# Optimization experiments

Measured on AMD Instinct MI355X. Metric: run time of the kernel, lower is better.

Reference implementation:

```python
import jax, jax.numpy as jnp
import numpy as np

B, N, D = 32, 64, 256

def _gelu(x):
    return jax.nn.gelu(x, approximate=False)

def setup_inputs() -> dict:
    key = jax.random.key(0)
    ks = jax.random.split(key, 16)
    def w(k, shape):
        fan_in = shape[0]
        return (jax.random.normal(k, shape, jnp.float32) / np.float32(np.sqrt(fan_in)))
    return {
        "dataset_embedding": jax.random.normal(ks[0], (B, D), jnp.float32),
        "variable_embeddings": jax.random.normal(ks[1], (B, N, D), jnp.float32),
        "claim_context": jax.random.normal(ks[2], (B, D), jnp.float32),
        "dge_w1": w(ks[3], (2 * D, D)), "dge_b1": jnp.zeros((D,), jnp.float32),
        "dge_w2": w(ks[4], (D, D)),     "dge_b2": jnp.zeros((D,), jnp.float32),
        "cge_w1": w(ks[5], (2 * D, D)), "cge_b1": jnp.zeros((D,), jnp.float32),
        "cge_w2": w(ks[6], (D, D)),     "cge_b2": jnp.zeros((D,), jnp.float32),
        "dep_w1": w(ks[7], (4 * D, D)), "dep_b1": jnp.zeros((D,), jnp.float32),
        "dep_w2": w(ks[8], (D, 1)),     "dep_b2": jnp.zeros((1,), jnp.float32),
        "cep_w1": w(ks[9], (4 * D, D)), "cep_b1": jnp.zeros((D,), jnp.float32),
        "cep_w2": w(ks[10], (D, 1)),    "cep_b2": jnp.zeros((1,), jnp.float32),
        "gate_w1": w(ks[11], (3, 64)),  "gate_b1": jnp.zeros((64,), jnp.float32),
        "gate_w2": w(ks[12], (64, 1)),  "gate_b2": jnp.zeros((1,), jnp.float32),
        "n_samples": 500,
    }

def _encode(ve, ctx, w1, b1, w2, b2):
    # Sequential(Linear(2d,d), GELU, Linear(d,d), GELU); dropout=0 (eval)
    x = jnp.concatenate([ve, jnp.broadcast_to(ctx[:, None, :], ve.shape)], axis=-1)
    h = _gelu(x @ w1 + b1)
    return _gelu(h @ w2 + b2)

def _predict_edges(ve_enc, ctx, w1, b1, w2, b2):
    # var_with_context: [B,N,2D]; edge features cat([var_i, var_j]) @ w1
    # == (vwc @ w1[:2D]) broadcast over i + (vwc @ w1[2D:]) broadcast over j
    vwc = jnp.concatenate([ve_enc, jnp.broadcast_to(ctx[:, None, :], ve_enc.shape)], axis=-1)
    wi, wj = w1[: 2 * D], w1[2 * D :]
    fi = vwc @ wi  # [B,N,D]
    fj = vwc @ wj  # [B,N,D]
    h = _gelu(fi[:, :, None, :] + fj[:, None, :, :] + b1)  # [B,N,N,D]
    logits = jnp.einsum("bijd,do->bij", h, w2) + b2[0]
    eye = jnp.eye(N, dtype=bool)
    return jnp.where(eye[None, :, :], jnp.float32(-1e9), logits)

def reference(dataset_embedding, variable_embeddings, claim_context,
              dge_w1, dge_b1, dge_w2, dge_b2,
              cge_w1, cge_b1, cge_w2, cge_b2,
              dep_w1, dep_b1, dep_w2, dep_b2,
              cep_w1, cep_b1, cep_w2, cep_b2,
              gate_w1, gate_b1, gate_w2, gate_b2,
              n_samples):
    avg_claim_confidence = 0.5
    var_data = _encode(variable_embeddings, dataset_embedding, dge_w1, dge_b1, dge_w2, dge_b2)
    var_claim = _encode(variable_embeddings, claim_context, cge_w1, cge_b1, cge_w2, cge_b2)
    W_data_logits = _predict_edges(var_data, dataset_embedding, dep_w1, dep_b1, dep_w2, dep_b2)
    W_claim_logits = _predict_edges(var_claim, claim_context, cep_w1, cep_b1, cep_w2, cep_b2)

    p = jax.nn.sigmoid(W_data_logits)
    eps = jnp.float32(1e-8)
    data_entropy = -(p * jnp.log(p + eps) + (1 - p) * jnp.log(1 - p + eps)).mean(axis=(1, 2))  # [B]

    ns = jnp.full((B,), min(n_samples / 1000.0, 1.0), jnp.float32)
    cc = jnp.full((B,), avg_claim_confidence, jnp.float32)
    gf = jnp.stack([ns, cc, data_entropy], axis=-1)  # [B,3]
    gate = jax.nn.sigmoid(_gelu(gf @ gate_w1 + gate_b1) @ gate_w2 + gate_b2)  # [B,1]
    gate = gate[:, :, None]  # [B,1,1]

    W_post_logits = gate * W_data_logits + (1 - gate) * W_claim_logits

    # NOTEARS: h(W) = tr(expm(W o W)) - n, W = sigmoid(logits)
    Wsig = jax.nn.sigmoid(W_post_logits)
    M = jax.vmap(jax.scipy.linalg.expm)(Wsig * Wsig)
    acyc = (jnp.trace(M, axis1=1, axis2=2) - N).mean()

    W_posterior = jax.nn.sigmoid(W_post_logits)
    return (W_posterior, acyc)
```

## Files before the change

### kernel.cpp

```cpp
#include <hip/hip_runtime.h>
#include <hip/hip_bf16.h>


#define LDS_STRIDE 260
#define ES 68

__device__ __forceinline__ float gelu_f(float x) {
    float z = fabsf(x) * 0.70710678118654752440f;
    float t = __builtin_amdgcn_rcpf(fmaf(0.3275911f, z, 1.0f));
    float p = t * fmaf(t, fmaf(t, fmaf(t, fmaf(t, 1.061405429f, -1.453152027f),
                                       1.421413741f), -0.284496736f), 0.254829592f);
    float e = __expf(-z * z);
    float erfv = fmaf(-p, e, 1.0f);
    erfv = copysignf(erfv, x);
    return 0.5f * x * (1.0f + erfv);
}
__device__ __forceinline__ float sigmoid_f(float x) {
    return 1.0f / (1.0f + expf(-x));
}
__device__ __forceinline__ float f4c(const float4& v, int k) {
    return k == 0 ? v.x : k == 1 ? v.y : k == 2 ? v.z : v.w;
}
__device__ __forceinline__ float4 ld4(const float* __restrict__ buf, int r, int c) {
    return *(const float4*)&buf[r * ES + c];
}

__global__ __launch_bounds__(256) void k0_ctx(
    const float* __restrict__ ds, const float* __restrict__ cc,
    const float* __restrict__ dge_w1, const float* __restrict__ dge_b1,
    const float* __restrict__ cge_w1, const float* __restrict__ cge_b1,
    const float* __restrict__ dep_w1, const float* __restrict__ dep_b1,
    const float* __restrict__ cep_w1, const float* __restrict__ cep_b1,
    float* __restrict__ ctxproj)
{
    const int b = blockIdx.x;
    const int which = blockIdx.y;
    const float* ctx; const float* W; const float* bias;
    switch (which) {
        case 0:  ctx = ds; W = dge_w1 + 256 * 256; bias = dge_b1; break;
        case 1:  ctx = cc; W = cge_w1 + 256 * 256; bias = cge_b1; break;
        case 2:  ctx = ds; W = dep_w1 + 256 * 256; bias = dep_b1; break;
        case 3:  ctx = ds; W = dep_w1 + 768 * 256; bias = nullptr; break;
        case 4:  ctx = cc; W = cep_w1 + 256 * 256; bias = cep_b1; break;
        default: ctx = cc; W = cep_w1 + 768 * 256; bias = nullptr; break;
    }
    __shared__ float sctx[256];
    const int tid = threadIdx.x;
    sctx[tid] = ctx[b * 256 + tid];
    __syncthreads();
    float acc = 0.0f;
    #pragma unroll 2
    for (int k = 0; k < 256; k += 4) {
        float4 c4 = *(const float4*)&sctx[k];
        acc = fmaf(c4.x, W[(k + 0) * 256 + tid], acc);
        acc = fmaf(c4.y, W[(k + 1) * 256 + tid], acc);
        acc = fmaf(c4.z, W[(k + 2) * 256 + tid], acc);
        acc = fmaf(c4.w, W[(k + 3) * 256 + tid], acc);
    }
    if (bias) acc += bias[tid];
    ctxproj[(which * 32 + b) * 256 + tid] = acc;
}

__device__ __forceinline__ void gemm_ks(const float* __restrict__ src,
                                        const float* __restrict__ W,
                                        int ks0, int t0, float acc[8][4])
{
    #pragma unroll
    for (int r = 0; r < 8; ++r)
        #pragma unroll
        for (int c = 0; c < 4; ++c) acc[r][c] = 0.0f;
    #pragma unroll 2
    for (int k = ks0; k < ks0 + 32; k += 4) {
        float4 wv0 = *(const float4*)&W[(k + 0) * 256 + t0];
        float4 wv1 = *(const float4*)&W[(k + 1) * 256 + t0];
        float4 wv2 = *(const float4*)&W[(k + 2) * 256 + t0];
        float4 wv3 = *(const float4*)&W[(k + 3) * 256 + t0];
        float4 a[8];
        #pragma unroll
        for (int r = 0; r < 8; ++r) a[r] = *(const float4*)&src[r * LDS_STRIDE + k];
        float4 wvs[4] = {wv0, wv1, wv2, wv3};
        #pragma unroll
        for (int kk = 0; kk < 4; ++kk) {
            float4 wv = wvs[kk];
            #pragma unroll
            for (int r = 0; r < 8; ++r) {
                float av = f4c(a[r], kk);
                acc[r][0] = fmaf(av, wv.x, acc[r][0]);
                acc[r][1] = fmaf(av, wv.y, acc[r][1]);
                acc[r][2] = fmaf(av, wv.z, acc[r][2]);
                acc[r][3] = fmaf(av, wv.w, acc[r][3]);
            }
        }
    }
}

__device__ __forceinline__ void part_write_rmw(float* __restrict__ part, int w, int t0,
                                               const float acc[8][4])
{
    if (w < 4) {
        #pragma unroll
        for (int r = 0; r < 8; ++r) {
            float4 o = {acc[r][0], acc[r][1], acc[r][2], acc[r][3]};
            *(float4*)&part[(w * 8 + r) * 256 + t0] = o;
        }
    }
    __syncthreads();
    if (w >= 4) {
        #pragma unroll
        for (int r = 0; r < 8; ++r) {
            float4 v = *(const float4*)&part[((w - 4) * 8 + r) * 256 + t0];
            float4 o = {v.x + acc[r][0], v.y + acc[r][1], v.z + acc[r][2], v.w + acc[r][3]};
            *(float4*)&part[((w - 4) * 8 + r) * 256 + t0] = o;
        }
    }
    __syncthreads();
}

__device__ __forceinline__ float4 reduce4(const float* __restrict__ part, int r, int t0)
{
    float4 s = {0.0f, 0.0f, 0.0f, 0.0f};
    #pragma unroll
    for (int sl = 0; sl < 4; ++sl) {
        float4 v = *(const float4*)&part[(sl * 8 + r) * 256 + t0];
        s.x += v.x; s.y += v.y; s.z += v.z; s.w += v.w;
    }
    return s;
}

__global__ __launch_bounds__(512, 4) void k1_encode(
    const float* __restrict__ ve_g,
    const float* __restrict__ dge_w1, const float* __restrict__ dge_w2, const float* __restrict__ dge_b2,
    const float* __restrict__ cge_w1, const float* __restrict__ cge_w2, const float* __restrict__ cge_b2,
    const float* __restrict__ dep_w1, const float* __restrict__ cep_w1,
    const float* __restrict__ ctxproj,
    float* __restrict__ fi_dep, float* __restrict__ fjt_dep,
    float* __restrict__ fi_cep, float* __restrict__ fjt_cep)
{
    __shared__ float sve[8 * LDS_STRIDE];
    __shared__ float sA[8 * LDS_STRIDE];
    __shared__ float sB[8 * LDS_STRIDE];
    __shared__ float part[4 * 8 * 256];

    const int tid   = threadIdx.x;
    const int blk   = blockIdx.x;
    const int chain = blk & 1;
    const int chunk = (blk >> 1) & 7;
    const int b     = blk >> 4;
    const int n0    = chunk * 8;

    const float* w1   = chain ? cge_w1 : dge_w1;
    const float* w2   = chain ? cge_w2 : dge_w2;
    const float* b2   = chain ? cge_b2 : dge_b2;
    const float* epw  = chain ? cep_w1 : dep_w1;
    float* fi  = chain ? fi_cep  : fi_dep;
    float* fjt = chain ? fjt_cep : fjt_dep;
    const int cp_s1 = chain ? 1 : 0;
    const int cp_fi = chain ? 4 : 2;
    const int cp_fj = chain ? 5 : 3;

    const int w  = tid >> 6;
    const int t0 = (tid & 63) * 4;
    const int ks0 = w * 32;

    float4 cp1 = *(const float4*)&ctxproj[(cp_s1 * 32 + b) * 256 + t0];
    float4 bv2 = *(const float4*)&b2[t0];
    float4 cpf = *(const float4*)&ctxproj[(cp_fi * 32 + b) * 256 + t0];
    float4 cpj = *(const float4*)&ctxproj[(cp_fj * 32 + b) * 256 + t0];

    {
        int idx = tid * 4;
        int r = idx >> 8, k = idx & 255;
        *(float4*)&sve[r * LDS_STRIDE + k] = *(const float4*)&ve_g[(b * 64 + n0) * 256 + idx];
    }
    __syncthreads();

    float acc[8][4];

    gemm_ks(sve, w1, ks0, t0, acc);
    part_write_rmw(part, w, t0, acc);
    {
        float4 s = reduce4(part, w, t0);
        float4 o = {gelu_f(s.x + cp1.x), gelu_f(s.y + cp1.y),
                    gelu_f(s.z + cp1.z), gelu_f(s.w + cp1.w)};
        *(float4*)&sA[w * LDS_STRIDE + t0] = o;
    }
    __syncthreads();

    gemm_ks(sA, w2, ks0, t0, acc);
    part_write_rmw(part, w, t0, acc);
    {
        float4 s = reduce4(part, w, t0);
        float4 o = {gelu_f(s.x + bv2.x), gelu_f(s.y + bv2.y),
                    gelu_f(s.z + bv2.z), gelu_f(s.w + bv2.w)};
        *(float4*)&sB[w * LDS_STRIDE + t0] = o;
    }
    __syncthreads();

    gemm_ks(sB, epw, ks0, t0, acc);
    part_write_rmw(part, w, t0, acc);
    {
        float4 s = reduce4(part, w, t0);
        float4 o = {s.x + cpf.x, s.y + cpf.y, s.z + cpf.z, s.w + cpf.w};
        *(float4*)&fi[(b * 64 + n0 + w) * 256 + t0] = o;
    }
    __syncthreads();

    gemm_ks(sB, epw + 512 * 256, ks0, t0, acc);
    part_write_rmw(part, w, t0, acc);
    {
        float4 s = reduce4(part, w, t0);
        float4 o = {s.x + cpj.x, s.y + cpj.y, s.z + cpj.z, s.w + cpj.w};
        *(float4*)&sA[w * LDS_STRIDE + t0] = o;
    }
    __syncthreads();
    {
        int t = tid & 255, half = tid >> 8;
        float v0 = sA[(half * 4 + 0) * LDS_STRIDE + t];
        float v1 = sA[(half * 4 + 1) * LDS_STRIDE + t];
        float v2 = sA[(half * 4 + 2) * LDS_STRIDE + t];
        float v3 = sA[(half * 4 + 3) * LDS_STRIDE + t];
        float4 o = {v0, v1, v2, v3};
        *(float4*)&fjt[(b * 256 + t) * 64 + n0 + half * 4] = o;
    }
}

__global__ __launch_bounds__(512) void k3_edges(
    const float* __restrict__ fi_dep, const float* __restrict__ fjt_dep,
    const float* __restrict__ fi_cep, const float* __restrict__ fjt_cep,
    const float* __restrict__ dep_w2, const float* __restrict__ dep_b2,
    const float* __restrict__ cep_w2, const float* __restrict__ cep_b2,
    float* __restrict__ Wd, float* __restrict__ Wc, float* __restrict__ entp)
{
    __shared__ float fj_s[2][64 * 64];
    __shared__ float fi_s[4][256];
    __shared__ float w2_s[256];
    __shared__ float red[8][64];

    const int blk  = blockIdx.x;
    const int pred = blk & 1;
    const int ig   = (blk >> 1) & 15;
    const int b    = blk >> 5;
    const int tid  = threadIdx.x;
    const int s    = tid >> 6;
    const int j    = tid & 63;
    const int row  = s & 3;
    const int dh   = s >> 2;

    const float* fi_g  = pred ? fi_cep  : fi_dep;
    const float* fjt_g = pred ? fjt_cep : fjt_dep;
    const float* w2_g  = pred ? cep_w2  : dep_w2;
    const float* b2_g  = pred ? cep_b2  : dep_b2;
    float* W_out = pred ? Wc : Wd;

    if (tid < 256) {
        int rr = tid >> 6, c = (tid & 63) * 4;
        *(float4*)&fi_s[rr][c] = *(const float4*)&fi_g[(b * 64 + ig * 4 + rr) * 256 + c];
    } else if (tid < 320) {
        int t = tid - 256;
        *(float4*)&w2_s[t * 4] = *(const float4*)&w2_g[t * 4];
    }

    const float4* gF = (const float4*)(fjt_g + b * 256 * 64);

    float4 r0 = gF[tid], r1 = gF[tid + 512];
    ((float4*)fj_s[0])[tid] = r0; ((float4*)fj_s[0])[tid + 512] = r1;
    __syncthreads();

    float acc = 0.0f;
    const int d0 = dh * 32;

    #pragma unroll
    for (int c = 0; c < 4; ++c) {
        const int p = c & 1;
        if (c < 3) {
            const int off = (c + 1) * 1024;
            r0 = gF[off + tid]; r1 = gF[off + tid + 512];
        }
        const float* fj = fj_s[p];
        const int c0 = c * 64;
        #pragma unroll 4
        for (int d = d0; d < d0 + 32; d += 2) {
            float f0 = fi_s[row][c0 + d];
            float f1 = fi_s[row][c0 + d + 1];
            float g0 = fj[(d + 0) * 64 + j];
            float g1 = fj[(d + 1) * 64 + j];
            acc = fmaf(gelu_f(f0 + g0), w2_s[c0 + d],     acc);
            acc = fmaf(gelu_f(f1 + g1), w2_s[c0 + d + 1], acc);
        }
        if (c < 3) {
            const int q = p ^ 1;
            ((float4*)fj_s[q])[tid] = r0; ((float4*)fj_s[q])[tid + 512] = r1;
            __syncthreads();
        }
    }

    red[s][j] = acc;
    __syncthreads();

    if (s < 4) {
        const int i = ig * 4 + s;
        float l = (red[s][j] + red[s + 4][j]) + b2_g[0];
        if (j == i) l = -1e9f;
        W_out[(b * 64 + i) * 64 + j] = l;

        if (pred == 0) {
            float p = sigmoid_f(l);
            float e = -(p * logf(p + 1e-8f) + (1.0f - p) * logf(1.0f - p + 1e-8f));
            #pragma unroll
            for (int off = 32; off; off >>= 1) e += __shfl_down(e, off);
            if (j == 0) entp[b * 64 + i] = e;
        }
    }
}

__device__ __forceinline__ void mm64f2(const float* __restrict__ A, const float* __restrict__ B,
                                       int r0, int c0, float acc[2][4])
{
    #pragma unroll
    for (int i = 0; i < 2; ++i)
        #pragma unroll
        for (int j = 0; j < 4; ++j) acc[i][j] = 0.0f;
    for (int kb = 0; kb < 64; kb += 4) {
        float4 a0 = ld4(A, r0 + 0, kb);
        float4 a1 = ld4(A, r0 + 1, kb);
        #pragma unroll
        for (int kk = 0; kk < 4; ++kk) {
            float4 rv = ld4(B, kb + kk, c0);
            float x0 = f4c(a0, kk), x1 = f4c(a1, kk);
            acc[0][0] = fmaf(x0, rv.x, acc[0][0]);
            acc[0][1] = fmaf(x0, rv.y, acc[0][1]);
            acc[0][2] = fmaf(x0, rv.z, acc[0][2]);
            acc[0][3] = fmaf(x0, rv.w, acc[0][3]);
            acc[1][0] = fmaf(x1, rv.x, acc[1][0]);
            acc[1][1] = fmaf(x1, rv.y, acc[1][1]);
            acc[1][2] = fmaf(x1, rv.z, acc[1][2]);
            acc[1][3] = fmaf(x1, rv.w, acc[1][3]);
        }
    }
}

__device__ __forceinline__ void mm64d2(const float* __restrict__ A, const float* __restrict__ B,
                                       int r0, int c0, double acc[2][4])
{
    #pragma unroll
    for (int i = 0; i < 2; ++i)
        #pragma unroll
        for (int j = 0; j < 4; ++j) acc[i][j] = 0.0;
    for (int kb = 0; kb < 64; kb += 4) {
        float4 a0 = ld4(A, r0 + 0, kb);
        float4 a1 = ld4(A, r0 + 1, kb);
        #pragma unroll
        for (int kk = 0; kk < 4; ++kk) {
            float4 rv = ld4(B, kb + kk, c0);
            double rj[4] = {(double)rv.x, (double)rv.y, (double)rv.z, (double)rv.w};
            double x0 = (double)f4c(a0, kk), x1 = (double)f4c(a1, kk);
            #pragma unroll
            for (int j = 0; j < 4; ++j) {
                acc[0][j] = fma(x0, rj[j], acc[0][j]);
                acc[1][j] = fma(x1, rj[j], acc[1][j]);
            }
        }
    }
}

__global__ __launch_bounds__(512) void k6_gate_expm(
    const float* __restrict__ Wd, const float* __restrict__ Wc,
    const float* __restrict__ entp,
    const float* __restrict__ gw1, const float* __restrict__ gb1,
    const float* __restrict__ gw2, const float* __restrict__ gb2,
    const int* __restrict__ n_samples,
    float* __restrict__ out, float* __restrict__ traces)
{
    __shared__ float Xs [64 * ES];
    __shared__ float X2s[64 * ES];
    __shared__ float X3s[64 * ES];
    __shared__ float Ra [64 * ES];
    __shared__ float Rb [64 * ES];
    __shared__ float sgate;
    __shared__ float sent;
    __shared__ int ssexp;

    const int b = blockIdx.x;
    const int tid = threadIdx.x;

    const float C2 = 0.5f, C3 = 1.0f/6.0f, C4 = 1.0f/24.0f, C5 = 1.0f/120.0f;
    const float C6 = 1.0f/720.0f, C7 = 1.0f/5040.0f, C8 = 1.0f/40320.0f;
    const float C9 = 1.0f/362880.0f, C10 = 1.0f/3628800.0f, C11 = 1.0f/39916800.0f;
    const float C12 = 1.0f/479001600.0f, C13 = 1.0f/6227020800.0f;

    if (tid < 64) {
        float v = entp[b * 64 + tid];
        #pragma unroll
        for (int off = 32; off; off >>= 1) v += __shfl_down(v, off);
        if (tid == 0) sent = v / 4096.0f;
    }
    __syncthreads();
    if (tid < 64) {
        float ns = fminf((float)n_samples[0] / 1000.0f, 1.0f);
        float ccf = 0.5f;
        float pre = ns * gw1[tid] + ccf * gw1[64 + tid] + sent * gw1[128 + tid] + gb1[tid];
        float hid = gelu_f(pre) * gw2[tid];
        #pragma unroll
        for (int off = 32; off; off >>= 1) hid += __shfl_down(hid, off);
        if (tid == 0) sgate = sigmoid_f(hid + gb2[0]);
    }
    __syncthreads();
    const float g = sgate;

    for (int idx = tid; idx < 4096; idx += 512) {
        float d = Wd[b * 4096 + idx];
        float c = Wc[b * 4096 + idx];
        float post = g * d + (1.0f - g) * c;
        float sg = sigmoid_f(post);
        out[b * 4096 + idx] = sg;
        Xs[(idx >> 6) * ES + (idx & 63)] = sg * sg;
    }
    __syncthreads();

    if (tid < 64) {
        float cs = 0.0f;
        for (int r = 0; r < 64; ++r) cs += Xs[r * ES + tid];
        #pragma unroll
        for (int off = 32; off; off >>= 1) cs = fmaxf(cs, __shfl_down(cs, off));
        if (tid == 0) {
            int se = 0;
            if (cs > 2.0f) se = (int)ceilf(log2f(cs * 0.5f));
            if (se < 0) se = 0;
            if (se > 12) se = 12;
            ssexp = se;
        }
    }
    __syncthreads();
    const int sexp = ssexp;
    const float scale = ldexpf(1.0f, -sexp);
    for (int idx = tid; idx < 4096; idx += 512) {
        Xs[(idx >> 6) * ES + (idx & 63)] *= scale;
    }
    __syncthreads();

    const int r0 = (tid >> 4) * 2;
    const int c0 = (tid & 15) * 4;
    float acc[2][4];

    mm64f2(Xs, Xs, r0, c0, acc);
    #pragma unroll
    for (int i = 0; i < 2; ++i) {
        float4 o = {acc[i][0], acc[i][1], acc[i][2], acc[i][3]};
        *(float4*)&X2s[(r0 + i) * ES + c0] = o;
    }
    __syncthreads();

    mm64f2(X2s, Xs, r0, c0, acc);
    #pragma unroll
    for (int i = 0; i < 2; ++i) {
        float4 o = {acc[i][0], acc[i][1], acc[i][2], acc[i][3]};
        *(float4*)&X3s[(r0 + i) * ES + c0] = o;
    }
    __syncthreads();

    mm64f2(Xs, X3s, r0, c0, acc);
    #pragma unroll
    for (int i = 0; i < 2; ++i) {
        float4 xv = ld4(Xs, r0 + i, c0);
        float4 x2 = ld4(X2s, r0 + i, c0);
        float4 x3 = ld4(X3s, r0 + i, c0);
        float o[4];
        #pragma unroll
        for (int j = 0; j < 4; ++j) {
            o[j] = C13 * acc[i][j] + C12 * f4c(x3, j) + C10 * f4c(xv, j) + C11 * f4c(x2, j)
                 + ((r0 + i) == (c0 + j) ? C9 : 0.0f);
        }
        float4 ov = {o[0], o[1], o[2], o[3]};
        *(float4*)&Ra[(r0 + i) * ES + c0] = ov;
    }
    __syncthreads();

    mm64f2(Ra, X3s, r0, c0, acc);
    #pragma unroll
    for (int i = 0; i < 2; ++i) {
        float4 xv = ld4(Xs, r0 + i, c0);
        float4 x2 = ld4(X2s, r0 + i, c0);
        float o[4];
        #pragma unroll
        for (int j = 0; j < 4; ++j) {
            o[j] = acc[i][j] + C7 * f4c(xv, j) + C8 * f4c(x2, j)
                 + ((r0 + i) == (c0 + j) ? C6 : 0.0f);
        }
        float4 ov = {o[0], o[1], o[2], o[3]};
        *(float4*)&Rb[(r0 + i) * ES + c0] = ov;
    }
    __syncthreads();

    mm64f2(Rb, X3s, r0, c0, acc);
    #pragma unroll
    for (int i = 0; i < 2; ++i) {
        float4 xv = ld4(Xs, r0 + i, c0);
        float4 x2 = ld4(X2s, r0 + i, c0);
        float o[4];
        #pragma unroll
        for (int j = 0; j < 4; ++j) {
            o[j] = acc[i][j] + C4 * f4c(xv, j) + C5 * f4c(x2, j)
                 + ((r0 + i) == (c0 + j) ? C3 : 0.0f);
        }
        float4 ov = {o[0], o[1], o[2], o[3]};
        *(float4*)&Ra[(r0 + i) * ES + c0] = ov;
    }
    __syncthreads();

    mm64f2(Ra, X3s, r0, c0, acc);
    #pragma unroll
    for (int i = 0; i < 2; ++i) {
        float4 xv = ld4(Xs, r0 + i, c0);
        float4 x2 = ld4(X2s, r0 + i, c0);
        float o[4];
        #pragma unroll
        for (int j = 0; j < 4; ++j) {
            o[j] = acc[i][j] + f4c(xv, j) + C2 * f4c(x2, j)
                 + ((r0 + i) == (c0 + j) ? 1.0f : 0.0f);
        }
        float4 ov = {o[0], o[1], o[2], o[3]};
        *(float4*)&Rb[(r0 + i) * ES + c0] = ov;
    }
    __syncthreads();

    float* cur = Rb;
    float* oth = Ra;
    for (int sq = 0; sq < sexp; ++sq) {
        double dacc[2][4];
        mm64d2(cur, cur, r0, c0, dacc);
        #pragma unroll
        for (int i = 0; i < 2; ++i) {
            float4 o = {(float)dacc[i][0], (float)dacc[i][1], (float)dacc[i][2], (float)dacc[i][3]};
            *(float4*)&oth[(r0 + i) * ES + c0] = o;
        }
        __syncthreads();
        float* t = cur; cur = oth; oth = t;
    }

    if (tid < 64) {
        double v = (double)cur[tid * ES + tid];
        #pragma unroll
        for (int off = 32; off; off >>= 1) v += __shfl_down(v, off);
        if (tid == 0) traces[b] = (float)v;
    }
}

__global__ void k7_acyc(const float* __restrict__ traces, float* __restrict__ out)
{
    if (threadIdx.x == 0 && blockIdx.x == 0) {
        double s = 0.0;
        for (int b = 0; b < 32; ++b) s += (double)traces[b];
        out[131072] = (float)(s / 32.0 - 64.0);
    }
}

extern "C" void kernel_launch(void* const* d_in, const int* in_sizes, int n_in,
                              void* d_out, int out_size, void* d_ws, size_t ws_size,
                              hipStream_t stream)
{
    (void)in_sizes; (void)n_in; (void)out_size; (void)ws_size;

    const float* ds     = (const float*)d_in[0];
    const float* ve     = (const float*)d_in[1];
    const float* cc     = (const float*)d_in[2];
    const float* dge_w1 = (const float*)d_in[3];
    const float* dge_b1 = (const float*)d_in[4];
    const float* dge_w2 = (const float*)d_in[5];
    const float* dge_b2 = (const float*)d_in[6];
    const float* cge_w1 = (const float*)d_in[7];
    const float* cge_b1 = (const float*)d_in[8];
    const float* cge_w2 = (const float*)d_in[9];
    const float* cge_b2 = (const float*)d_in[10];
    const float* dep_w1 = (const float*)d_in[11];
    const float* dep_b1 = (const float*)d_in[12];
    const float* dep_w2 = (const float*)d_in[13];
    const float* dep_b2 = (const float*)d_in[14];
    const float* cep_w1 = (const float*)d_in[15];
    const float* cep_b1 = (const float*)d_in[16];
    const float* cep_w2 = (const float*)d_in[17];
    const float* cep_b2 = (const float*)d_in[18];
    const float* gw1    = (const float*)d_in[19];
    const float* gb1    = (const float*)d_in[20];
    const float* gw2    = (const float*)d_in[21];
    const float* gb2    = (const float*)d_in[22];
    const int*   nsamp  = (const int*)d_in[23];

    float* ws = (float*)d_ws;
    float* ctxproj = ws;
    float* fi_dep  = ctxproj + 49152;
    float* fjt_dep = fi_dep + 524288;
    float* fi_cep  = fjt_dep + 524288;
    float* fjt_cep = fi_cep + 524288;
    float* Wd      = fjt_cep + 524288;
    float* Wc      = Wd + 131072;
    float* entp    = Wc + 131072;
    float* traces  = entp + 2048;

    float* outp = (float*)d_out;

    k0_ctx<<<dim3(32, 6), 256, 0, stream>>>(ds, cc, dge_w1, dge_b1, cge_w1, cge_b1,
                                            dep_w1, dep_b1, cep_w1, cep_b1, ctxproj);
    k1_encode<<<512, 512, 0, stream>>>(ve, dge_w1, dge_w2, dge_b2,
                                       cge_w1, cge_w2, cge_b2,
                                       dep_w1, cep_w1, ctxproj,
                                       fi_dep, fjt_dep, fi_cep, fjt_cep);
    k3_edges<<<1024, 512, 0, stream>>>(fi_dep, fjt_dep, fi_cep, fjt_cep,
                                       dep_w2, dep_b2, cep_w2, cep_b2,
                                       Wd, Wc, entp);
    k6_gate_expm<<<32, 512, 0, stream>>>(Wd, Wc, entp, gw1, gb1, gw2, gb2,
                                         nsamp, outp, traces);
    k7_acyc<<<1, 64, 0, stream>>>(traces, outp);
}
```

Measured before the change: 120.8 us.

## Replace split-K encode GEMM with per-thread full-K output tiling

```diff
diff --git a/kernel.cpp b/kernel.cpp
--- a/kernel.cpp
+++ b/kernel.cpp
@@ -61,70 +61,35 @@
     ctxproj[(which * 32 + b) * 256 + tid] = acc;
 }
 
-__device__ __forceinline__ void gemm_ks(const float* __restrict__ src,
+__device__ __forceinline__ void gemm_cs(const float* __restrict__ src,
                                         const float* __restrict__ W,
-                                        int ks0, int t0, float acc[8][4])
-{
-    #pragma unroll
-    for (int r = 0; r < 8; ++r)
-        #pragma unroll
-        for (int c = 0; c < 4; ++c) acc[r][c] = 0.0f;
+                                        int r, int c0, float acc[4])
+{
+    acc[0] = acc[1] = acc[2] = acc[3] = 0.0f;
     #pragma unroll 2
-    for (int k = ks0; k < ks0 + 32; k += 4) {
-        float4 wv0 = *(const float4*)&W[(k + 0) * 256 + t0];
-        float4 wv1 = *(const float4*)&W[(k + 1) * 256 + t0];
-        float4 wv2 = *(const float4*)&W[(k + 2) * 256 + t0];
-        float4 wv3 = *(const float4*)&W[(k + 3) * 256 + t0];
-        float4 a[8];
-        #pragma unroll
-        for (int r = 0; r < 8; ++r) a[r] = *(const float4*)&src[r * LDS_STRIDE + k];
-        float4 wvs[4] = {wv0, wv1, wv2, wv3};
-        #pragma unroll
-        for (int kk = 0; kk < 4; ++kk) {
-            float4 wv = wvs[kk];
-            #pragma unroll
-            for (int r = 0; r < 8; ++r) {
-                float av = f4c(a[r], kk);
-                acc[r][0] = fmaf(av, wv.x, acc[r][0]);
-                acc[r][1] = fmaf(av, wv.y, acc[r][1]);
-                acc[r][2] = fmaf(av, wv.z, acc[r][2]);
-                acc[r][3] = fmaf(av, wv.w, acc[r][3]);
-            }
-        }
-    }
-}
-
-__device__ __forceinline__ void part_write_rmw(float* __restrict__ part, int w, int t0,
-                                               const float acc[8][4])
-{
-    if (w < 4) {
-        #pragma unroll
-        for (int r = 0; r < 8; ++r) {
-            float4 o = {acc[r][0], acc[r][1], acc[r][2], acc[r][3]};
-            *(float4*)&part[(w * 8 + r) * 256 + t0] = o;
-        }
-    }
-    __syncthreads();
-    if (w >= 4) {
-        #pragma unroll
-        for (int r = 0; r < 8; ++r) {
-            float4 v = *(const float4*)&part[((w - 4) * 8 + r) * 256 + t0];
-            float4 o = {v.x + acc[r][0], v.y + acc[r][1], v.z + acc[r][2], v.w + acc[r][3]};
-            *(float4*)&part[((w - 4) * 8 + r) * 256 + t0] = o;
-        }
-    }
-    __syncthreads();
-}
-
-__device__ __forceinline__ float4 reduce4(const float* __restrict__ part, int r, int t0)
-{
-    float4 s = {0.0f, 0.0f, 0.0f, 0.0f};
-    #pragma unroll
-    for (int sl = 0; sl < 4; ++sl) {
-        float4 v = *(const float4*)&part[(sl * 8 + r) * 256 + t0];
-        s.x += v.x; s.y += v.y; s.z += v.z; s.w += v.w;
-    }
-    return s;
+    for (int k = 0; k < 256; k += 4) {
+        float4 a  = *(const float4*)&src[r * LDS_STRIDE + k];
+        float4 w0 = *(const float4*)&W[(k + 0) * 256 + c0];
+        float4 w1 = *(const float4*)&W[(k + 1) * 256 + c0];
+        float4 w2 = *(const float4*)&W[(k + 2) * 256 + c0];
+        float4 w3 = *(const float4*)&W[(k + 3) * 256 + c0];
+        acc[0] = fmaf(a.x, w0.x, acc[0]);
+        acc[1] = fmaf(a.x, w0.y, acc[1]);
+        acc[2] = fmaf(a.x, w0.z, acc[2]);
+        acc[3] = fmaf(a.x, w0.w, acc[3]);
+        acc[0] = fmaf(a.y, w1.x, acc[0]);
+        acc[1] = fmaf(a.y, w1.y, acc[1]);
+        acc[2] = fmaf(a.y, w1.z, acc[2]);
+        acc[3] = fmaf(a.y, w1.w, acc[3]);
+        acc[0] = fmaf(a.z, w2.x, acc[0]);
+        acc[1] = fmaf(a.z, w2.y, acc[1]);
+        acc[2] = fmaf(a.z, w2.z, acc[2]);
+        acc[3] = fmaf(a.z, w2.w, acc[3]);
+        acc[0] = fmaf(a.w, w3.x, acc[0]);
+        acc[1] = fmaf(a.w, w3.y, acc[1]);
+        acc[2] = fmaf(a.w, w3.z, acc[2]);
+        acc[3] = fmaf(a.w, w3.w, acc[3]);
+    }
 }
 
 __global__ __launch_bounds__(512, 4) void k1_encode(
@@ -139,7 +104,6 @@
     __shared__ float sve[8 * LDS_STRIDE];
     __shared__ float sA[8 * LDS_STRIDE];
     __shared__ float sB[8 * LDS_STRIDE];
-    __shared__ float part[4 * 8 * 256];
 
     const int tid   = threadIdx.x;
     const int blk   = blockIdx.x;
@@ -159,60 +123,53 @@
     const int cp_fj = chain ? 5 : 3;
 
     const int w  = tid >> 6;
-    const int t0 = (tid & 63) * 4;
-    const int ks0 = w * 32;
-
-    float4 cp1 = *(const float4*)&ctxproj[(cp_s1 * 32 + b) * 256 + t0];
-    float4 bv2 = *(const float4*)&b2[t0];
-    float4 cpf = *(const float4*)&ctxproj[(cp_fi * 32 + b) * 256 + t0];
-    float4 cpj = *(const float4*)&ctxproj[(cp_fj * 32 + b) * 256 + t0];
+    const int l  = tid & 63;
+    const int r  = l >> 3;
+    const int c0 = w * 32 + (l & 7) * 4;
+
+    float4 cp1 = *(const float4*)&ctxproj[(cp_s1 * 32 + b) * 256 + c0];
+    float4 bv2 = *(const float4*)&b2[c0];
+    float4 cpf = *(const float4*)&ctxproj[(cp_fi * 32 + b) * 256 + c0];
+    float4 cpj = *(const float4*)&ctxproj[(cp_fj * 32 + b) * 256 + c0];
 
     {
         int idx = tid * 4;
-        int r = idx >> 8, k = idx & 255;
-        *(float4*)&sve[r * LDS_STRIDE + k] = *(const float4*)&ve_g[(b * 64 + n0) * 256 + idx];
-    }
-    __syncthreads();
-
-    float acc[8][4];
-
-    gemm_ks(sve, w1, ks0, t0, acc);
-    part_write_rmw(part, w, t0, acc);
+        int rr = idx >> 8, k = idx & 255;
+        *(float4*)&sve[rr * LDS_STRIDE + k] = *(const float4*)&ve_g[(b * 64 + n0) * 256 + idx];
+    }
+    __syncthreads();
+
+    float acc[4];
+
+    gemm_cs(sve, w1, r, c0, acc);
     {
-        float4 s = reduce4(part, w, t0);
-        float4 o = {gelu_f(s.x + cp1.x), gelu_f(s.y + cp1.y),
-                    gelu_f(s.z + cp1.z), gelu_f(s.w + cp1.w)};
-        *(float4*)&sA[w * LDS_STRIDE + t0] = o;
-    }
-    __syncthreads();
-
-    gemm_ks(sA, w2, ks0, t0, acc);
-    part_write_rmw(part, w, t0, acc);
+        float4 o = {gelu_f(acc[0] + cp1.x), gelu_f(acc[1] + cp1.y),
+                    gelu_f(acc[2] + cp1.z), gelu_f(acc[3] + cp1.w)};
+        *(float4*)&sA[r * LDS_STRIDE + c0] = o;
+    }
+    __syncthreads();
+
+    gemm_cs(sA, w2, r, c0, acc);
     {
-        float4 s = reduce4(part, w, t0);
-        float4 o = {gelu_f(s.x + bv2.x), gelu_f(s.y + bv2.y),
-                    gelu_f(s.z + bv2.z), gelu_f(s.w + bv2.w)};
-        *(float4*)&sB[w * LDS_STRIDE + t0] = o;
-    }
-    __syncthreads();
-
-    gemm_ks(sB, epw, ks0, t0, acc);
-    part_write_rmw(part, w, t0, acc);
+        float4 o = {gelu_f(acc[0] + bv2.x), gelu_f(acc[1] + bv2.y),
+                    gelu_f(acc[2] + bv2.z), gelu_f(acc[3] + bv2.w)};
+        *(float4*)&sB[r * LDS_STRIDE + c0] = o;
+    }
+    __syncthreads();
+
+    gemm_cs(sB, epw, r, c0, acc);
     {
-        float4 s = reduce4(part, w, t0);
-        float4 o = {s.x + cpf.x, s.y + cpf.y, s.z + cpf.z, s.w + cpf.w};
-        *(float4*)&fi[(b * 64 + n0 + w) * 256 + t0] = o;
-    }
-    __syncthreads();
-
-    gemm_ks(sB, epw + 512 * 256, ks0, t0, acc);
-    part_write_rmw(part, w, t0, acc);
+        float4 o = {acc[0] + cpf.x, acc[1] + cpf.y, acc[2] + cpf.z, acc[3] + cpf.w};
+        *(float4*)&fi[(b * 64 + n0 + r) * 256 + c0] = o;
+    }
+
+    gemm_cs(sB, epw + 512 * 256, r, c0, acc);
     {
-        float4 s = reduce4(part, w, t0);
-        float4 o = {s.x + cpj.x, s.y + cpj.y, s.z + cpj.z, s.w + cpj.w};
-        *(float4*)&sA[w * LDS_STRIDE + t0] = o;
-    }
-    __syncthreads();
+        float4 o = {acc[0] + cpj.x, acc[1] + cpj.y, acc[2] + cpj.z, acc[3] + cpj.w};
+        *(float4*)&sA[r * LDS_STRIDE + c0] = o;
+    }
+    __syncthreads();
+
     {
         int t = tid & 255, half = tid >> 8;
         float v0 = sA[(half * 4 + 0) * LDS_STRIDE + t];
```

New measurement: 203.7 us. 1.69x slower.
